# Performance work log

Hardware: AMD Instinct MI355X
Metric: run time of the kernel (lower is better)

Reference implementation:

```python
import jax, jax.numpy as jnp
import numpy as np

NUM_USERS = 100000
NUM_ITEMS = 50000
EMB_DIM = 64
NUM_EDGES = 2000000


def setup_inputs() -> dict:
    key = jax.random.key(0)
    k1, k2, k3, k4 = jax.random.split(key, 4)
    user_table = jax.random.normal(k1, (NUM_USERS, EMB_DIM), dtype=jnp.float32) * 0.1
    item_table = jax.random.normal(k2, (NUM_ITEMS, EMB_DIM), dtype=jnp.float32) * 0.1
    user_idx = jax.random.randint(k3, (NUM_EDGES,), 0, NUM_USERS, dtype=jnp.int32)
    item_idx = jax.random.randint(k4, (NUM_EDGES,), 0, NUM_ITEMS, dtype=jnp.int32)
    return {"user_table": user_table, "item_table": item_table,
            "user_idx": user_idx, "item_idx": item_idx, "num_layers": 3}


def reference(user_table, item_table, user_idx, item_idx, num_layers):
    """LightGCN-style k-hop propagation over a sparse bipartite user-item graph.

    A_hat[u,i] = 1/sqrt(deg_u * deg_i); emb_out = mean over hops 0..K of A_hat^k @ emb_0.
    Returns concatenated [num_users+num_items, d] embeddings (forward() then slices).
    """
    n_users, d = user_table.shape
    n_items = item_table.shape[0]
    ones = jnp.ones(user_idx.shape[0], dtype=user_table.dtype)
    deg_u = jax.ops.segment_sum(ones, user_idx, num_segments=n_users)
    deg_i = jax.ops.segment_sum(ones, item_idx, num_segments=n_items)
    deg_u = jnp.where(deg_u > 0, deg_u, 1.0)
    deg_i = jnp.where(deg_i > 0, deg_i, 1.0)
    # per-edge symmetric normalization coefficient [E]
    norm = jax.lax.rsqrt(deg_u[user_idx] * deg_i[item_idx])

    u, it = user_table, item_table
    acc_u, acc_i = u, it
    for _ in range(num_layers):
        # messages: item -> user and user -> item (gather + weighted scatter-add)
        msg_u = jax.ops.segment_sum(norm[:, None] * it[item_idx], user_idx, num_segments=n_users)
        msg_i = jax.ops.segment_sum(norm[:, None] * u[user_idx], item_idx, num_segments=n_items)
        u, it = msg_u, msg_i
        acc_u = acc_u + u
        acc_i = acc_i + it
    scale = 1.0 / (num_layers + 1)
    return jnp.concatenate([acc_u * scale, acc_i * scale], axis=0)
```

## Files before the change

### kernel.cpp

```cpp
#include <hip/hip_runtime.h>
#include <hip/hip_fp16.h>
#include <stdint.h>

#define NU 100000
#define NI 50000
#define NN (NU + NI)
#define DIM 64
#define NE 2000000
#define TOT (NN * DIM)

#define BEPT 8
#define BCHUNK (256 * BEPT)
#define BGRID ((NE + BCHUNK - 1) / BCHUNK)

#define NBU 782
#define NBI 782
#define NBKT (NBU + NBI)
#define SCAP 3064
#define NBRMASK 0x3FFFF

typedef float f4v __attribute__((ext_vector_type(4)));
typedef float f2v __attribute__((ext_vector_type(2)));

__device__ __forceinline__ int bucket_of(int dst) {
    return (dst < NU) ? (dst >> 7) : (NBU + ((dst - NU) >> 6));
}
__device__ __forceinline__ int bucket_r0(int b) {
    return (b < NBU) ? (b << 7) : (NU + ((b - NBU) << 6));
}


__global__ void bin_kernel(const int* __restrict__ uidx, const int* __restrict__ iidx,
                           int* __restrict__ bktcur, uint32_t* __restrict__ stg) {
    __shared__ int cnt[NBKT];
    __shared__ int base[NBKT + 1];
    __shared__ int gbase[NBKT];
    __shared__ int partial[256];
    __shared__ uint64_t rec[2 * BCHUNK];
    int tid = threadIdx.x;
    for (int i = tid; i < NBKT; i += 256) cnt[i] = 0;
    __syncthreads();

    int t0 = blockIdx.x * BCHUNK + tid;
    int dsts[2 * BEPT], nbs[2 * BEPT], bks[2 * BEPT], rks[2 * BEPT];
#pragma unroll
    for (int k = 0; k < BEPT; ++k) {
        int e = t0 + k * 256;
        bool ok = e < NE;
        int u = ok ? __builtin_nontemporal_load(uidx + e) : 0;
        int it = ok ? NU + __builtin_nontemporal_load(iidx + e) : 0;
        dsts[2 * k] = u;    nbs[2 * k] = it;   bks[2 * k] = ok ? bucket_of(u) : -1;
        dsts[2 * k + 1] = it; nbs[2 * k + 1] = u; bks[2 * k + 1] = ok ? bucket_of(it) : -1;
    }
#pragma unroll
    for (int k = 0; k < 2 * BEPT; ++k)
        rks[k] = (bks[k] >= 0) ? atomicAdd(&cnt[bks[k]], 1) : 0;
    __syncthreads();

    int s = 0;
    int b0 = tid * 7;
#pragma unroll
    for (int k = 0; k < 7; ++k) { int i = b0 + k; if (i < NBKT) s += cnt[i]; }
    partial[tid] = s;
    __syncthreads();
    for (int off = 1; off < 256; off <<= 1) {
        int v = (tid >= off) ? partial[tid - off] : 0;
        __syncthreads();
        partial[tid] += v;
        __syncthreads();
    }
    int excl = (tid == 0) ? 0 : partial[tid - 1];
#pragma unroll
    for (int k = 0; k < 7; ++k) {
        int i = b0 + k;
        if (i < NBKT) { base[i] = excl; excl += cnt[i]; }
    }
    if (tid == 255) base[NBKT] = partial[255];
    __syncthreads();

    for (int i = tid; i < NBKT; i += 256)
        if (cnt[i] > 0) gbase[i] = atomicAdd(&bktcur[i], cnt[i]);
#pragma unroll
    for (int k = 0; k < 2 * BEPT; ++k)
        if (bks[k] >= 0)
            rec[base[bks[k]] + rks[k]] = ((uint64_t)(uint32_t)nbs[k] << 32) | (uint32_t)dsts[k];
    __syncthreads();

    int T = base[NBKT];
    for (int p = tid; p < T; p += 256) {
        uint64_t r = rec[p];
        int dst = (int)(uint32_t)r;
        int nbr = (int)(uint32_t)(r >> 32);
        int b = bucket_of(dst);
        int pos = gbase[b] + (p - base[b]);
        uint32_t packed = ((uint32_t)(dst - bucket_r0(b)) << 18) | (uint32_t)nbr;
        if (pos < SCAP)
            __builtin_nontemporal_store(packed, stg + (size_t)b * SCAP + pos);
    }
}

__global__ void placeA_kernel(const int* __restrict__ bktcnt, const uint32_t* __restrict__ stg,
                              int* __restrict__ deg) {
    __shared__ int rowcnt[128];
    int b = blockIdx.x;
    int tid = threadIdx.x;
    int r0 = bucket_r0(b);
    int r1 = (b < NBU) ? min(r0 + 128, NU) : min(r0 + 64, NN);
    int nrows = r1 - r0;
    if (tid < nrows) rowcnt[tid] = 0;
    __syncthreads();
    int n = min(bktcnt[b], SCAP);
    const uint32_t* run = stg + (size_t)b * SCAP;
    for (int p = tid; p < n; p += 256) {
        uint32_t r = __builtin_nontemporal_load(run + p);
        atomicAdd(&rowcnt[r >> 18], 1);
    }
    __syncthreads();
    if (tid < nrows) deg[r0 + tid] = rowcnt[tid];
}

__global__ void scan1_kernel(const int* __restrict__ deg, int* __restrict__ incl,
                             int* __restrict__ bsum) {
    __shared__ int tmp[256];
    int i = blockIdx.x * 256 + threadIdx.x;
    int v = (i < NN) ? deg[i] : 0;
    tmp[threadIdx.x] = v;
    __syncthreads();
    for (int off = 1; off < 256; off <<= 1) {
        int t = (threadIdx.x >= off) ? tmp[threadIdx.x - off] : 0;
        __syncthreads();
        tmp[threadIdx.x] += t;
        __syncthreads();
    }
    if (i < NN) incl[i] = tmp[threadIdx.x];
    if (threadIdx.x == 255) bsum[blockIdx.x] = tmp[255];
}

__global__ void scan2_kernel(int* __restrict__ bsum, int nb) {
    __shared__ int tmp[1024];
    int v = (threadIdx.x < nb) ? bsum[threadIdx.x] : 0;
    tmp[threadIdx.x] = v;
    __syncthreads();
    for (int off = 1; off < 1024; off <<= 1) {
        int t = (threadIdx.x >= off) ? tmp[threadIdx.x - off] : 0;
        __syncthreads();
        tmp[threadIdx.x] += t;
        __syncthreads();
    }
    if (threadIdx.x < nb) bsum[threadIdx.x] = tmp[threadIdx.x] - v;
}

__global__ void scan3_kernel(const int* __restrict__ deg, const int* __restrict__ incl,
                             const int* __restrict__ bsum,
                             int* __restrict__ rowptr, float* __restrict__ rdeg,
                             float* __restrict__ irdeg) {
    int i = blockIdx.x * 256 + threadIdx.x;
    if (i >= NN) return;
    int inc = incl[i] + bsum[blockIdx.x];
    rowptr[i + 1] = inc;
    int d = deg[i];
    rdeg[i] = (d > 0) ? rsqrtf((float)d) : 1.0f;
    irdeg[i] = (d > 0) ? sqrtf((float)d) : 1.0f;
    if (i == 0) rowptr[0] = 0;
}

__global__ void placeB_kernel(const int* __restrict__ rowptr, const int* __restrict__ bktcnt,
                              const uint32_t* __restrict__ stg, int* __restrict__ nbrs) {
    __shared__ int rptr[129];
    __shared__ int rowcnt[128];
    __shared__ int outb[SCAP];
    int b = blockIdx.x;
    int tid = threadIdx.x;
    int r0 = bucket_r0(b);
    int r1 = (b < NBU) ? min(r0 + 128, NU) : min(r0 + 64, NN);
    int nrows = r1 - r0;
    if (tid <= nrows) rptr[tid] = rowptr[r0 + tid];
    if (tid < nrows) rowcnt[tid] = 0;
    __syncthreads();
    int lo = rptr[0];
    int n = min(bktcnt[b], SCAP);
    const uint32_t* run = stg + (size_t)b * SCAP;
    for (int p = tid; p < n; p += 256) {
        uint32_t r = __builtin_nontemporal_load(run + p);
        int row = r >> 18;
        int rk = atomicAdd(&rowcnt[row], 1);
        outb[rptr[row] - lo + rk] = (int)(r & NBRMASK);
    }
    __syncthreads();
    int nseg = rptr[nrows] - lo;
    for (int i = tid; i < nseg; i += 256)
        __builtin_nontemporal_store(outb[i], nbrs + lo + i);
}


__global__ void initsrc_kernel(const float* __restrict__ ut, const float* __restrict__ it,
                               const float* __restrict__ rdeg, __half* __restrict__ srcH) {
    int i = blockIdx.x * blockDim.x + threadIdx.x;
    const int NU4 = NU * DIM / 4;
    const int T4 = TOT / 4;
    if (i >= T4) return;
    float4 v = (i < NU4) ? ((const float4*)ut)[i] : ((const float4*)it)[i - NU4];
    float r = rdeg[i >> 4];
    union { __half2 h2[2]; f2v v2; } u;
    u.h2[0] = __floats2half2_rn(r * v.x, r * v.y);
    u.h2[1] = __floats2half2_rn(r * v.z, r * v.w);
    *((f2v*)(srcH + (size_t)i * 4)) = u.v2;
}

__global__ void gather_kernel(const int* __restrict__ rowptr, const int* __restrict__ nbrs,
                              const float* __restrict__ rdeg,
                              const __half* __restrict__ srcH,
                              __half* __restrict__ nxtH, int prescale) {
    int wid = (int)(((unsigned)blockIdx.x * blockDim.x + threadIdx.x) >> 6);
    if (wid >= NN) return;
    int lane = threadIdx.x & 63;
    int g = lane >> 3;
    int c = lane & 7;
    int start = rowptr[wid];
    int end = rowptr[wid + 1];
    int deg = end - start;

    int nb_l = (lane < deg) ? __builtin_nontemporal_load(nbrs + start + lane) : 0;

    float s0=0,s1=0,s2=0,s3=0,s4=0,s5=0,s6=0,s7=0;
    int dmain = deg < 64 ? deg : 64;
    int iters = (dmain + 7) >> 3;
    for (int t = 0; t < iters; ++t) {
        int idx = t * 8 + g;
        int nb = __shfl(nb_l, idx & 63, 64);
        bool ok = idx < dmain;
        if (!ok) nb = 0;
        union { f4v v; __half2 h2[4]; } u;
        u.v = *((const f4v*)(srcH + (size_t)nb * DIM) + c);
        if (ok) {
            float2 f0 = __half22float2(u.h2[0]);
            float2 f1 = __half22float2(u.h2[1]);
            float2 f2 = __half22float2(u.h2[2]);
            float2 f3 = __half22float2(u.h2[3]);
            s0 += f0.x; s1 += f0.y; s2 += f1.x; s3 += f1.y;
            s4 += f2.x; s5 += f2.y; s6 += f3.x; s7 += f3.y;
        }
    }
    for (int k = start + 64 + g; k < end; k += 8) {
        int nb = nbrs[k];
        union { f4v v; __half2 h2[4]; } u;
        u.v = *((const f4v*)(srcH + (size_t)nb * DIM) + c);
        float2 f0 = __half22float2(u.h2[0]);
        float2 f1 = __half22float2(u.h2[1]);
        float2 f2 = __half22float2(u.h2[2]);
        float2 f3 = __half22float2(u.h2[3]);
        s0 += f0.x; s1 += f0.y; s2 += f1.x; s3 += f1.y;
        s4 += f2.x; s5 += f2.y; s6 += f3.x; s7 += f3.y;
    }

#pragma unroll
    for (int mask = 8; mask <= 32; mask <<= 1) {
        s0 += __shfl_xor(s0, mask, 64); s1 += __shfl_xor(s1, mask, 64);
        s2 += __shfl_xor(s2, mask, 64); s3 += __shfl_xor(s3, mask, 64);
        s4 += __shfl_xor(s4, mask, 64); s5 += __shfl_xor(s5, mask, 64);
        s6 += __shfl_xor(s6, mask, 64); s7 += __shfl_xor(s7, mask, 64);
    }

    if (lane < 8) {
        float r = rdeg[wid];
        float w = prescale ? r * r : r;
        union { f4v v; __half2 h2[4]; } o;
        o.h2[0] = __floats2half2_rn(w * s0, w * s1);
        o.h2[1] = __floats2half2_rn(w * s2, w * s3);
        o.h2[2] = __floats2half2_rn(w * s4, w * s5);
        o.h2[3] = __floats2half2_rn(w * s6, w * s7);
        __builtin_nontemporal_store(o.v, (f4v*)(nxtH + (size_t)wid * DIM + c * 8));
    }
}

__global__ void combine_kernel(const float* __restrict__ ut, const float* __restrict__ it,
                               const float* __restrict__ irdeg,
                               const __half* __restrict__ n1, const __half* __restrict__ n2,
                               const __half* __restrict__ n3, float* __restrict__ acc) {
    int i = blockIdx.x * blockDim.x + threadIdx.x;
    const int T8 = TOT / 8;
    if (i >= T8) return;
    int row = i >> 3;
    float w = irdeg[row];
    const int NU8 = NU * DIM / 8;
    const float* e0 = (i < NU8) ? (ut + (size_t)i * 8) : (it + (size_t)(i - NU8) * 8);
    f4v ea = ((const f4v*)e0)[0];
    f4v eb = ((const f4v*)e0)[1];
    union { f4v v; __half2 h2[4]; } a1, a2, a3;
    a1.v = __builtin_nontemporal_load((const f4v*)n1 + i);
    a2.v = __builtin_nontemporal_load((const f4v*)n2 + i);
    a3.v = __builtin_nontemporal_load((const f4v*)n3 + i);
    f4v oa, ob;
    {
        float2 f1 = __half22float2(a1.h2[0]), f2 = __half22float2(a2.h2[0]), f3 = __half22float2(a3.h2[0]);
        oa.x = 0.25f * (ea.x + w * (f1.x + f2.x) + f3.x);
        oa.y = 0.25f * (ea.y + w * (f1.y + f2.y) + f3.y);
        f1 = __half22float2(a1.h2[1]); f2 = __half22float2(a2.h2[1]); f3 = __half22float2(a3.h2[1]);
        oa.z = 0.25f * (ea.z + w * (f1.x + f2.x) + f3.x);
        oa.w = 0.25f * (ea.w + w * (f1.y + f2.y) + f3.y);
        f1 = __half22float2(a1.h2[2]); f2 = __half22float2(a2.h2[2]); f3 = __half22float2(a3.h2[2]);
        ob.x = 0.25f * (eb.x + w * (f1.x + f2.x) + f3.x);
        ob.y = 0.25f * (eb.y + w * (f1.y + f2.y) + f3.y);
        f1 = __half22float2(a1.h2[3]); f2 = __half22float2(a2.h2[3]); f3 = __half22float2(a3.h2[3]);
        ob.z = 0.25f * (eb.z + w * (f1.x + f2.x) + f3.x);
        ob.w = 0.25f * (eb.w + w * (f1.y + f2.y) + f3.y);
    }
    __builtin_nontemporal_store(oa, (f4v*)(acc + (size_t)i * 8));
    __builtin_nontemporal_store(ob, (f4v*)(acc + (size_t)i * 8) + 1);
}

extern "C" void kernel_launch(void* const* d_in, const int* in_sizes, int n_in,
                              void* d_out, int out_size, void* d_ws, size_t ws_size,
                              hipStream_t stream) {
    const float* ut = (const float*)d_in[0];
    const float* it = (const float*)d_in[1];
    const int* uidx = (const int*)d_in[2];
    const int* iidx = (const int*)d_in[3];

    float* acc = (float*)d_out;

    int* wsi = (int*)d_ws;
    int* deg    = wsi;
    int* incl   = deg + NN;
    int* rowptr = incl + NN;
    int* bsum   = rowptr + (NN + 1);
    float* rdeg = (float*)(bsum + 1024);
    float* irdeg = rdeg + NN;
    int* bktcur = (int*)(irdeg + NN);
    size_t off = (size_t)((int*)(bktcur + NBKT) - wsi);
    off = (off + 15) & ~(size_t)15;
    int* nbrs   = wsi + off;
    __half* bufA = (__half*)(nbrs + 2 * (size_t)NE);
    __half* bufB = bufA + (size_t)TOT;
    __half* bufC = bufB + (size_t)TOT;
    uint32_t* stg = (uint32_t*)bufA;

    const int B = 256;
    const int nb = (NN + 255) / 256;

    hipMemsetAsync(bktcur, 0, sizeof(int) * NBKT, stream);
    bin_kernel<<<BGRID, 256, 0, stream>>>(uidx, iidx, bktcur, stg);
    placeA_kernel<<<NBKT, 256, 0, stream>>>(bktcur, stg, deg);
    scan1_kernel<<<nb, 256, 0, stream>>>(deg, incl, bsum);
    scan2_kernel<<<1, 1024, 0, stream>>>(bsum, nb);
    scan3_kernel<<<nb, 256, 0, stream>>>(deg, incl, bsum, rowptr, rdeg, irdeg);
    placeB_kernel<<<NBKT, 256, 0, stream>>>(rowptr, bktcur, stg, nbrs);

    initsrc_kernel<<<(TOT / 4 + B - 1) / B, B, 0, stream>>>(ut, it, rdeg, bufA);

    const int gblocks = NN / 4;
    gather_kernel<<<gblocks, B, 0, stream>>>(rowptr, nbrs, rdeg, bufA, bufB, 1);
    gather_kernel<<<gblocks, B, 0, stream>>>(rowptr, nbrs, rdeg, bufB, bufC, 1);
    gather_kernel<<<gblocks, B, 0, stream>>>(rowptr, nbrs, rdeg, bufC, bufA, 0);
    combine_kernel<<<(TOT / 8 + B - 1) / B, B, 0, stream>>>(ut, it, irdeg, bufB, bufC, bufA, acc);
}
```

Baseline: 472.9 us.

## Split edge binning into two-level radix passes and fuse last gather with combine

Replaces the single-pass binning into 1564 buckets with a two-level scheme: a first pass bins edges into 63 coarse groups, then a second pass splits each group into 25 fine buckets. This is meant to cut shared-memory scan and scatter overhead. It also merges the third propagation layer with the final combine, so the last layer's half-precision buffer is never written out and read back. The cost is an extra kernel launch and an extra staging round trip for the edge records.

Result: faster. 416.3 us (-12.0%).

```diff
diff --git a/kernel.cpp b/kernel.cpp
--- a/kernel.cpp
+++ b/kernel.cpp
@@ -9,93 +9,132 @@
 #define NE 2000000
 #define TOT (NN * DIM)
 
-#define BEPT 8
-#define BCHUNK (256 * BEPT)
-#define BGRID ((NE + BCHUNK - 1) / BCHUNK)
-
 #define NBU 782
 #define NBI 782
 #define NBKT (NBU + NBI)
 #define SCAP 3064
-#define NBRMASK 0x3FFFF
+#define CGRP 25
+#define NC 63
+#define CCAP 67584
+
+#define BEPT1 4
+#define BCH1 (256 * BEPT1)
+#define BG1 ((NE + BCH1 - 1) / BCH1)
+#define KB2 17
 
 typedef float f4v __attribute__((ext_vector_type(4)));
 typedef float f2v __attribute__((ext_vector_type(2)));
 
-__device__ __forceinline__ int bucket_of(int dst) {
-    return (dst < NU) ? (dst >> 7) : (NBU + ((dst - NU) >> 6));
-}
 __device__ __forceinline__ int bucket_r0(int b) {
     return (b < NBU) ? (b << 7) : (NU + ((b - NBU) << 6));
 }
 
 
-__global__ void bin_kernel(const int* __restrict__ uidx, const int* __restrict__ iidx,
-                           int* __restrict__ bktcur, uint32_t* __restrict__ stg) {
-    __shared__ int cnt[NBKT];
-    __shared__ int base[NBKT + 1];
-    __shared__ int gbase[NBKT];
-    __shared__ int partial[256];
-    __shared__ uint64_t rec[2 * BCHUNK];
+__global__ void bin1_kernel(const int* __restrict__ uidx, const int* __restrict__ iidx,
+                            int* __restrict__ ccur, uint32_t* __restrict__ cstg) {
+    __shared__ int cnt[NC];
+    __shared__ int base[NC + 1];
+    __shared__ int gbase[NC];
+    __shared__ uint32_t rec[2 * BCH1];
+    __shared__ uint8_t cid[2 * BCH1];
     int tid = threadIdx.x;
-    for (int i = tid; i < NBKT; i += 256) cnt[i] = 0;
-    __syncthreads();
-
-    int t0 = blockIdx.x * BCHUNK + tid;
-    int dsts[2 * BEPT], nbs[2 * BEPT], bks[2 * BEPT], rks[2 * BEPT];
-#pragma unroll
-    for (int k = 0; k < BEPT; ++k) {
+    for (int i = tid; i < NC; i += 256) cnt[i] = 0;
+    __syncthreads();
+
+    uint32_t pk[2 * BEPT1]; int cs[2 * BEPT1]; int rk[2 * BEPT1];
+    int t0 = blockIdx.x * BCH1 + tid;
+#pragma unroll
+    for (int k = 0; k < BEPT1; ++k) {
         int e = t0 + k * 256;
         bool ok = e < NE;
         int u = ok ? __builtin_nontemporal_load(uidx + e) : 0;
-        int it = ok ? NU + __builtin_nontemporal_load(iidx + e) : 0;
-        dsts[2 * k] = u;    nbs[2 * k] = it;   bks[2 * k] = ok ? bucket_of(u) : -1;
-        dsts[2 * k + 1] = it; nbs[2 * k + 1] = u; bks[2 * k + 1] = ok ? bucket_of(it) : -1;
-    }
-#pragma unroll
-    for (int k = 0; k < 2 * BEPT; ++k)
-        rks[k] = (bks[k] >= 0) ? atomicAdd(&cnt[bks[k]], 1) : 0;
-    __syncthreads();
-
-    int s = 0;
-    int b0 = tid * 7;
-#pragma unroll
-    for (int k = 0; k < 7; ++k) { int i = b0 + k; if (i < NBKT) s += cnt[i]; }
-    partial[tid] = s;
-    __syncthreads();
-    for (int off = 1; off < 256; off <<= 1) {
-        int v = (tid >= off) ? partial[tid - off] : 0;
-        __syncthreads();
-        partial[tid] += v;
-        __syncthreads();
-    }
-    int excl = (tid == 0) ? 0 : partial[tid - 1];
-#pragma unroll
-    for (int k = 0; k < 7; ++k) {
-        int i = b0 + k;
-        if (i < NBKT) { base[i] = excl; excl += cnt[i]; }
-    }
-    if (tid == 255) base[NBKT] = partial[255];
-    __syncthreads();
-
-    for (int i = tid; i < NBKT; i += 256)
-        if (cnt[i] > 0) gbase[i] = atomicAdd(&bktcur[i], cnt[i]);
-#pragma unroll
-    for (int k = 0; k < 2 * BEPT; ++k)
-        if (bks[k] >= 0)
-            rec[base[bks[k]] + rks[k]] = ((uint64_t)(uint32_t)nbs[k] << 32) | (uint32_t)dsts[k];
-    __syncthreads();
-
-    int T = base[NBKT];
+        int itm = ok ? __builtin_nontemporal_load(iidx + e) : 0;
+        int b = u >> 7; int c = b / 25; int f5 = b - c * 25;
+        pk[2 * k] = ((uint32_t)f5 << 23) | ((uint32_t)(u & 127) << 16) | (uint32_t)itm;
+        cs[2 * k] = ok ? c : -1;
+        int b2 = NBU + (itm >> 6); int c2 = b2 / 25; int f52 = b2 - c2 * 25;
+        pk[2 * k + 1] = ((uint32_t)f52 << 23) | ((uint32_t)(itm & 63) << 17) | (uint32_t)u;
+        cs[2 * k + 1] = ok ? c2 : -1;
+    }
+#pragma unroll
+    for (int k = 0; k < 2 * BEPT1; ++k)
+        rk[k] = (cs[k] >= 0) ? atomicAdd(&cnt[cs[k]], 1) : 0;
+    __syncthreads();
+    if (tid == 0) {
+        int s = 0;
+        for (int i = 0; i < NC; ++i) { base[i] = s; s += cnt[i]; }
+        base[NC] = s;
+    }
+    __syncthreads();
+    for (int i = tid; i < NC; i += 256)
+        if (cnt[i] > 0) gbase[i] = atomicAdd(&ccur[i], cnt[i]);
+#pragma unroll
+    for (int k = 0; k < 2 * BEPT1; ++k)
+        if (cs[k] >= 0) {
+            int p = base[cs[k]] + rk[k];
+            rec[p] = pk[k];
+            cid[p] = (uint8_t)cs[k];
+        }
+    __syncthreads();
+    int T = base[NC];
     for (int p = tid; p < T; p += 256) {
-        uint64_t r = rec[p];
-        int dst = (int)(uint32_t)r;
-        int nbr = (int)(uint32_t)(r >> 32);
-        int b = bucket_of(dst);
-        int pos = gbase[b] + (p - base[b]);
-        uint32_t packed = ((uint32_t)(dst - bucket_r0(b)) << 18) | (uint32_t)nbr;
+        int c = cid[p];
+        int pos = gbase[c] + (p - base[c]);
+        if (pos < CCAP)
+            __builtin_nontemporal_store(rec[p], cstg + (size_t)c * CCAP + pos);
+    }
+}
+
+__global__ void bin2_kernel(const int* __restrict__ ccnt, const uint32_t* __restrict__ cstg,
+                            int* __restrict__ bktcur, uint32_t* __restrict__ stg) {
+    int c = blockIdx.x / KB2;
+    int sl = blockIdx.x % KB2;
+    int n = min(ccnt[c], CCAP);
+    int lo = sl * 4096;
+    if (lo >= n) return;
+    int hi = min(lo + 4096, n);
+    int m = hi - lo;
+    __shared__ int cnt[CGRP];
+    __shared__ int base[CGRP + 1];
+    __shared__ int gbase[CGRP];
+    __shared__ uint32_t rec[4096];
+    int tid = threadIdx.x;
+    if (tid < CGRP) cnt[tid] = 0;
+    __syncthreads();
+
+    uint32_t pk[16]; int fa[16]; int rk[16];
+    const uint32_t* run = cstg + (size_t)c * CCAP + lo;
+#pragma unroll
+    for (int k = 0; k < 16; ++k) {
+        int p = tid + k * 256;
+        bool ok = p < m;
+        uint32_t r = ok ? __builtin_nontemporal_load(run + p) : 0;
+        pk[k] = r;
+        fa[k] = ok ? (int)(r >> 23) : -1;
+    }
+#pragma unroll
+    for (int k = 0; k < 16; ++k)
+        rk[k] = (fa[k] >= 0) ? atomicAdd(&cnt[fa[k]], 1) : 0;
+    __syncthreads();
+    if (tid == 0) {
+        int s = 0;
+        for (int i = 0; i < CGRP; ++i) { base[i] = s; s += cnt[i]; }
+        base[CGRP] = s;
+    }
+    __syncthreads();
+    if (tid < CGRP && cnt[tid] > 0)
+        gbase[tid] = atomicAdd(&bktcur[c * CGRP + tid], cnt[tid]);
+#pragma unroll
+    for (int k = 0; k < 16; ++k)
+        if (fa[k] >= 0) rec[base[fa[k]] + rk[k]] = pk[k];
+    __syncthreads();
+    int T = base[CGRP];
+    for (int p = tid; p < T; p += 256) {
+        uint32_t r = rec[p];
+        int f5 = r >> 23;
+        int pos = gbase[f5] + (p - base[f5]);
         if (pos < SCAP)
-            __builtin_nontemporal_store(packed, stg + (size_t)b * SCAP + pos);
+            __builtin_nontemporal_store(r, stg + (size_t)(c * CGRP + f5) * SCAP + pos);
     }
 }
 
@@ -111,9 +150,11 @@
     __syncthreads();
     int n = min(bktcnt[b], SCAP);
     const uint32_t* run = stg + (size_t)b * SCAP;
+    bool isU = b < NBU;
     for (int p = tid; p < n; p += 256) {
         uint32_t r = __builtin_nontemporal_load(run + p);
-        atomicAdd(&rowcnt[r >> 18], 1);
+        int row = isU ? ((r >> 16) & 0x7F) : ((r >> 17) & 0x3F);
+        atomicAdd(&rowcnt[row], 1);
     }
     __syncthreads();
     if (tid < nrows) deg[r0 + tid] = rowcnt[tid];
@@ -180,11 +221,13 @@
     int lo = rptr[0];
     int n = min(bktcnt[b], SCAP);
     const uint32_t* run = stg + (size_t)b * SCAP;
+    bool isU = b < NBU;
     for (int p = tid; p < n; p += 256) {
         uint32_t r = __builtin_nontemporal_load(run + p);
-        int row = r >> 18;
+        int row = isU ? ((r >> 16) & 0x7F) : ((r >> 17) & 0x3F);
+        int nbr = isU ? (NU + (int)(r & 0xFFFF)) : (int)(r & 0x1FFFF);
         int rk = atomicAdd(&rowcnt[row], 1);
-        outb[rptr[row] - lo + rk] = (int)(r & NBRMASK);
+        outb[rptr[row] - lo + rk] = nbr;
     }
     __syncthreads();
     int nseg = rptr[nrows] - lo;
@@ -209,8 +252,7 @@
 
 __global__ void gather_kernel(const int* __restrict__ rowptr, const int* __restrict__ nbrs,
                               const float* __restrict__ rdeg,
-                              const __half* __restrict__ srcH,
-                              __half* __restrict__ nxtH, int prescale) {
+                              const __half* __restrict__ srcH, __half* __restrict__ nxtH) {
     int wid = (int)(((unsigned)blockIdx.x * blockDim.x + threadIdx.x) >> 6);
     if (wid >= NN) return;
     int lane = threadIdx.x & 63;
@@ -252,7 +294,6 @@
         s0 += f0.x; s1 += f0.y; s2 += f1.x; s3 += f1.y;
         s4 += f2.x; s5 += f2.y; s6 += f3.x; s7 += f3.y;
     }
-
 #pragma unroll
     for (int mask = 8; mask <= 32; mask <<= 1) {
         s0 += __shfl_xor(s0, mask, 64); s1 += __shfl_xor(s1, mask, 64);
@@ -260,10 +301,9 @@
         s4 += __shfl_xor(s4, mask, 64); s5 += __shfl_xor(s5, mask, 64);
         s6 += __shfl_xor(s6, mask, 64); s7 += __shfl_xor(s7, mask, 64);
     }
-
     if (lane < 8) {
         float r = rdeg[wid];
-        float w = prescale ? r * r : r;
+        float w = r * r;
         union { f4v v; __half2 h2[4]; } o;
         o.h2[0] = __floats2half2_rn(w * s0, w * s1);
         o.h2[1] = __floats2half2_rn(w * s2, w * s3);
@@ -273,40 +313,87 @@
     }
 }
 
-__global__ void combine_kernel(const float* __restrict__ ut, const float* __restrict__ it,
-                               const float* __restrict__ irdeg,
-                               const __half* __restrict__ n1, const __half* __restrict__ n2,
-                               const __half* __restrict__ n3, float* __restrict__ acc) {
-    int i = blockIdx.x * blockDim.x + threadIdx.x;
-    const int T8 = TOT / 8;
-    if (i >= T8) return;
-    int row = i >> 3;
-    float w = irdeg[row];
-    const int NU8 = NU * DIM / 8;
-    const float* e0 = (i < NU8) ? (ut + (size_t)i * 8) : (it + (size_t)(i - NU8) * 8);
-    f4v ea = ((const f4v*)e0)[0];
-    f4v eb = ((const f4v*)e0)[1];
-    union { f4v v; __half2 h2[4]; } a1, a2, a3;
-    a1.v = __builtin_nontemporal_load((const f4v*)n1 + i);
-    a2.v = __builtin_nontemporal_load((const f4v*)n2 + i);
-    a3.v = __builtin_nontemporal_load((const f4v*)n3 + i);
-    f4v oa, ob;
-    {
-        float2 f1 = __half22float2(a1.h2[0]), f2 = __half22float2(a2.h2[0]), f3 = __half22float2(a3.h2[0]);
-        oa.x = 0.25f * (ea.x + w * (f1.x + f2.x) + f3.x);
-        oa.y = 0.25f * (ea.y + w * (f1.y + f2.y) + f3.y);
-        f1 = __half22float2(a1.h2[1]); f2 = __half22float2(a2.h2[1]); f3 = __half22float2(a3.h2[1]);
-        oa.z = 0.25f * (ea.z + w * (f1.x + f2.x) + f3.x);
-        oa.w = 0.25f * (ea.w + w * (f1.y + f2.y) + f3.y);
-        f1 = __half22float2(a1.h2[2]); f2 = __half22float2(a2.h2[2]); f3 = __half22float2(a3.h2[2]);
-        ob.x = 0.25f * (eb.x + w * (f1.x + f2.x) + f3.x);
-        ob.y = 0.25f * (eb.y + w * (f1.y + f2.y) + f3.y);
-        f1 = __half22float2(a1.h2[3]); f2 = __half22float2(a2.h2[3]); f3 = __half22float2(a3.h2[3]);
-        ob.z = 0.25f * (eb.z + w * (f1.x + f2.x) + f3.x);
-        ob.w = 0.25f * (eb.w + w * (f1.y + f2.y) + f3.y);
-    }
-    __builtin_nontemporal_store(oa, (f4v*)(acc + (size_t)i * 8));
-    __builtin_nontemporal_store(ob, (f4v*)(acc + (size_t)i * 8) + 1);
+__global__ void gather_fused_kernel(const int* __restrict__ rowptr, const int* __restrict__ nbrs,
+                                    const float* __restrict__ rdeg, const float* __restrict__ irdeg,
+                                    const __half* __restrict__ srcH,
+                                    const __half* __restrict__ n1, const __half* __restrict__ n2,
+                                    const float* __restrict__ ut, const float* __restrict__ it,
+                                    float* __restrict__ acc) {
+    int wid = (int)(((unsigned)blockIdx.x * blockDim.x + threadIdx.x) >> 6);
+    if (wid >= NN) return;
+    int lane = threadIdx.x & 63;
+    int g = lane >> 3;
+    int c = lane & 7;
+    int start = rowptr[wid];
+    int end = rowptr[wid + 1];
+    int deg = end - start;
+
+    int nb_l = (lane < deg) ? __builtin_nontemporal_load(nbrs + start + lane) : 0;
+
+    float s0=0,s1=0,s2=0,s3=0,s4=0,s5=0,s6=0,s7=0;
+    int dmain = deg < 64 ? deg : 64;
+    int iters = (dmain + 7) >> 3;
+    for (int t = 0; t < iters; ++t) {
+        int idx = t * 8 + g;
+        int nb = __shfl(nb_l, idx & 63, 64);
+        bool ok = idx < dmain;
+        if (!ok) nb = 0;
+        union { f4v v; __half2 h2[4]; } u;
+        u.v = *((const f4v*)(srcH + (size_t)nb * DIM) + c);
+        if (ok) {
+            float2 f0 = __half22float2(u.h2[0]);
+            float2 f1 = __half22float2(u.h2[1]);
+            float2 f2 = __half22float2(u.h2[2]);
+            float2 f3 = __half22float2(u.h2[3]);
+            s0 += f0.x; s1 += f0.y; s2 += f1.x; s3 += f1.y;
+            s4 += f2.x; s5 += f2.y; s6 += f3.x; s7 += f3.y;
+        }
+    }
+    for (int k = start + 64 + g; k < end; k += 8) {
+        int nb = nbrs[k];
+        union { f4v v; __half2 h2[4]; } u;
+        u.v = *((const f4v*)(srcH + (size_t)nb * DIM) + c);
+        float2 f0 = __half22float2(u.h2[0]);
+        float2 f1 = __half22float2(u.h2[1]);
+        float2 f2 = __half22float2(u.h2[2]);
+        float2 f3 = __half22float2(u.h2[3]);
+        s0 += f0.x; s1 += f0.y; s2 += f1.x; s3 += f1.y;
+        s4 += f2.x; s5 += f2.y; s6 += f3.x; s7 += f3.y;
+    }
+#pragma unroll
+    for (int mask = 8; mask <= 32; mask <<= 1) {
+        s0 += __shfl_xor(s0, mask, 64); s1 += __shfl_xor(s1, mask, 64);
+        s2 += __shfl_xor(s2, mask, 64); s3 += __shfl_xor(s3, mask, 64);
+        s4 += __shfl_xor(s4, mask, 64); s5 += __shfl_xor(s5, mask, 64);
+        s6 += __shfl_xor(s6, mask, 64); s7 += __shfl_xor(s7, mask, 64);
+    }
+    if (lane < 8) {
+        float r = rdeg[wid];
+        float w = irdeg[wid];
+        const float* e0 = ((wid < NU) ? (ut + (size_t)wid * DIM)
+                                      : (it + (size_t)(wid - NU) * DIM)) + c * 8;
+        f4v ea = ((const f4v*)e0)[0];
+        f4v eb = ((const f4v*)e0)[1];
+        union { f4v v; __half2 h2[4]; } a1, a2;
+        size_t ro = (size_t)wid * DIM + c * 8;
+        a1.v = __builtin_nontemporal_load((const f4v*)(n1 + ro));
+        a2.v = __builtin_nontemporal_load((const f4v*)(n2 + ro));
+        f4v oa, ob;
+        float2 f1 = __half22float2(a1.h2[0]), f2 = __half22float2(a2.h2[0]);
+        oa.x = 0.25f * (ea.x + w * (f1.x + f2.x) + r * s0);
+        oa.y = 0.25f * (ea.y + w * (f1.y + f2.y) + r * s1);
+        f1 = __half22float2(a1.h2[1]); f2 = __half22float2(a2.h2[1]);
+        oa.z = 0.25f * (ea.z + w * (f1.x + f2.x) + r * s2);
+        oa.w = 0.25f * (ea.w + w * (f1.y + f2.y) + r * s3);
+        f1 = __half22float2(a1.h2[2]); f2 = __half22float2(a2.h2[2]);
+        ob.x = 0.25f * (eb.x + w * (f1.x + f2.x) + r * s4);
+        ob.y = 0.25f * (eb.y + w * (f1.y + f2.y) + r * s5);
+        f1 = __half22float2(a1.h2[3]); f2 = __half22float2(a2.h2[3]);
+        ob.z = 0.25f * (eb.z + w * (f1.x + f2.x) + r * s6);
+        ob.w = 0.25f * (eb.w + w * (f1.y + f2.y) + r * s7);
+        __builtin_nontemporal_store(oa, (f4v*)(acc + ro));
+        __builtin_nontemporal_store(ob, (f4v*)(acc + ro) + 1);
+    }
 }
 
 extern "C" void kernel_launch(void* const* d_in, const int* in_sizes, int n_in,
@@ -327,19 +414,22 @@
     float* rdeg = (float*)(bsum + 1024);
     float* irdeg = rdeg + NN;
     int* bktcur = (int*)(irdeg + NN);
-    size_t off = (size_t)((int*)(bktcur + NBKT) - wsi);
+    int* ccur   = bktcur + NBKT;
+    size_t off = (size_t)((int*)(ccur + NC) - wsi);
     off = (off + 15) & ~(size_t)15;
     int* nbrs   = wsi + off;
     __half* bufA = (__half*)(nbrs + 2 * (size_t)NE);
     __half* bufB = bufA + (size_t)TOT;
     __half* bufC = bufB + (size_t)TOT;
-    uint32_t* stg = (uint32_t*)bufA;
+    uint32_t* stg  = (uint32_t*)bufA;
+    uint32_t* cstg = (uint32_t*)bufB;
 
     const int B = 256;
     const int nb = (NN + 255) / 256;
 
-    hipMemsetAsync(bktcur, 0, sizeof(int) * NBKT, stream);
-    bin_kernel<<<BGRID, 256, 0, stream>>>(uidx, iidx, bktcur, stg);
+    hipMemsetAsync(bktcur, 0, sizeof(int) * (NBKT + NC), stream);
+    bin1_kernel<<<BG1, 256, 0, stream>>>(uidx, iidx, ccur, cstg);
+    bin2_kernel<<<NC * KB2, 256, 0, stream>>>(ccur, cstg, bktcur, stg);
     placeA_kernel<<<NBKT, 256, 0, stream>>>(bktcur, stg, deg);
     scan1_kernel<<<nb, 256, 0, stream>>>(deg, incl, bsum);
     scan2_kernel<<<1, 1024, 0, stream>>>(bsum, nb);
@@ -349,8 +439,8 @@
     initsrc_kernel<<<(TOT / 4 + B - 1) / B, B, 0, stream>>>(ut, it, rdeg, bufA);
 
     const int gblocks = NN / 4;
-    gather_kernel<<<gblocks, B, 0, stream>>>(rowptr, nbrs, rdeg, bufA, bufB, 1);
-    gather_kernel<<<gblocks, B, 0, stream>>>(rowptr, nbrs, rdeg, bufB, bufC, 1);
-    gather_kernel<<<gblocks, B, 0, stream>>>(rowptr, nbrs, rdeg, bufC, bufA, 0);
-    combine_kernel<<<(TOT / 8 + B - 1) / B, B, 0, stream>>>(ut, it, irdeg, bufB, bufC, bufA, acc);
-}
+    gather_kernel<<<gblocks, B, 0, stream>>>(rowptr, nbrs, rdeg, bufA, bufB);
+    gather_kernel<<<gblocks, B, 0, stream>>>(rowptr, nbrs, rdeg, bufB, bufC);
+    gather_fused_kernel<<<gblocks, B, 0, stream>>>(rowptr, nbrs, rdeg, irdeg,
+                                                   bufC, bufB, bufC, ut, it, acc);
+}
```
